# Kernel tuning notes

Hardware: AMD Instinct MI355X
Metric: run time of the kernel (lower is better)

The kernel has to match this reference:

```python
import jax, jax.numpy as jnp
import numpy as np

K = 3   # num nearest neighbors (init k)
P = 2   # IDW power (init p)


def setup_inputs() -> dict:
    key = jax.random.key(0)
    k1, k2, k3, k4 = jax.random.split(key, 4)
    B, N, M, C = 8, 16384, 1024, 256
    xyz = jax.random.normal(k1, (B, N, 3), dtype=jnp.float32)
    sampled_xyz = jax.random.normal(k2, (B, M, 3), dtype=jnp.float32)
    sampled_features = jax.random.normal(k3, (B, M, C), dtype=jnp.float32)
    masks = jax.random.randint(k4, (B, N), 0, 2, dtype=jnp.int32)
    return {"xyz": xyz, "sampled_xyz": sampled_xyz,
            "sampled_features": sampled_features, "masks": masks}


def reference(xyz, sampled_xyz, sampled_features, masks):
    # xyz: [B,N,3], sampled_xyz: [B,M,3], sampled_features: [B,M,C], masks: [B,N]
    # Squared pairwise distances [B,N,M] (same math as the chunked torch loop).
    delta = xyz[:, :, None, :] - sampled_xyz[:, None, :, :]
    dists = jnp.sum(delta * delta, axis=-1)
    # k smallest distances -> negate and take top-k.
    neg_top, idx = jax.lax.top_k(-dists, K)          # [B,N,K]
    min_dists = jnp.maximum(-neg_top, 1e-10)
    weights = 1.0 / (min_dists ** P + 1e-10)
    weights = weights / jnp.sum(weights, axis=-1, keepdims=True)
    # Gather neighbor features: [B,N,K,C]
    gathered = jax.vmap(lambda f, i: f[i])(sampled_features, idx)
    interpolated = jnp.sum(gathered * weights[..., None], axis=2)  # [B,N,C]
    # Invalid (masked-out) rows stay zero, matching the padded scatter.
    valid = (masks != 0).astype(interpolated.dtype)
    return interpolated * valid[..., None]
```

## Files before the change

### kernel.cpp

```cpp
#include <hip/hip_runtime.h>

constexpr int B = 8;
constexpr int N = 16384;
constexpr int M = 1024;
constexpr int C = 256;
constexpr int QW = 4;

typedef float vf16 __attribute__((ext_vector_type(16)));

__global__ __launch_bounds__(256, 8) void upsample_idw_kernel(
    const float* __restrict__ xyz,
    const float* __restrict__ sxyz,
    const float* __restrict__ feats,
    const int*   __restrict__ masks,
    float*       __restrict__ out)
{
    const int tid = threadIdx.x;
    const int w   = tid >> 6;
    const int l   = tid & 63;
    const int blk = blockIdx.x;
    const int b     = blk & 7;
    const int nbase = (blk >> 3) << 7;

    __shared__ unsigned long long s_key[2][64][QW][3];
    __shared__ float s_wt[2][64][3];
    __shared__ int   s_j[2][64][4];

    const float* bbase = sxyz + (size_t)b * (M * 3);
    const int qoff = __builtin_amdgcn_readfirstlane((tid >> 6) * (256 * 12));

    const float* xp0 = xyz + ((size_t)b * N + nbase + l) * 3;
    const float* xp1 = xyz + ((size_t)b * N + nbase + 64 + l) * 3;
    const float x0 = xp0[0], y0 = xp0[1], z0 = xp0[2];
    const float x1 = xp1[0], y1 = xp1[1], z1 = xp1[2];

    const float4* Fb4 = (const float4*)(feats + (size_t)b * (M * C));
    float4* op40 = (float4*)(out + (((size_t)b * N + nbase) * C));
    float4* op41 = (float4*)(out + (((size_t)b * N + nbase + 64) * C));

    auto scan_chunk = [&](int ch, float px, float py, float pz,
                          float& d0, float& d1, float& d2,
                          int& i0, int& i1, int& i2) {
        vf16 ca, cb, cc;
        const int off = qoff + ch * 192;
        asm volatile(
            "s_load_dwordx16 %0, %3, %4\n\t"
            "s_load_dwordx16 %1, %3, %4 offset:64\n\t"
            "s_load_dwordx16 %2, %3, %4 offset:128\n\t"
            "s_waitcnt lgkmcnt(0)"
            : "=&s"(ca), "=&s"(cb), "=&s"(cc)
            : "s"(bbase), "s"(off));
        #pragma unroll
        for (int j = 0; j < 16; ++j) {
            const int f0 = 3 * j, f1 = 3 * j + 1, f2 = 3 * j + 2;
            const float cx = (f0 < 16) ? ca[f0 & 15] : (f0 < 32) ? cb[f0 & 15] : cc[f0 & 15];
            const float cy = (f1 < 16) ? ca[f1 & 15] : (f1 < 32) ? cb[f1 & 15] : cc[f1 & 15];
            const float cz = (f2 < 16) ? ca[f2 & 15] : (f2 < 32) ? cb[f2 & 15] : cc[f2 & 15];
            const float dx = __fsub_rn(cx, px);
            const float dy = __fsub_rn(cy, py);
            const float dz = __fsub_rn(cz, pz);
            const float d  = __fadd_rn(__fadd_rn(__fmul_rn(dx, dx), __fmul_rn(dy, dy)),
                                       __fmul_rn(dz, dz));
            const int m = ch * 16 + j;
            const bool lt0 = d < d0, lt1 = d < d1, lt2 = d < d2;
            i2 = lt1 ? i1 : (lt2 ? m : i2);
            i1 = lt0 ? i0 : (lt1 ? m : i1);
            i0 = lt0 ? m  : i0;
            const float nd2 = __builtin_amdgcn_fmed3f(d1, d2, d);
            const float nd1 = __builtin_amdgcn_fmed3f(d0, d1, d);
            d2 = nd2; d1 = nd1; d0 = fminf(d0, d);
        }
    };

    auto store_keys = [&](int t, float d0, float d1, float d2,
                          int i0, int i1, int i2) {
        const unsigned base = (unsigned)(w * 256);
        s_key[t][l][w][0] = ((unsigned long long)__float_as_uint(d0) << 32) | (base + (unsigned)i0);
        s_key[t][l][w][1] = ((unsigned long long)__float_as_uint(d1) << 32) | (base + (unsigned)i1);
        s_key[t][l][w][2] = ((unsigned long long)__float_as_uint(d2) << 32) | (base + (unsigned)i2);
    };

    auto merge = [&](int t) {
        if (tid < 64) {
            unsigned long long k0 = ~0ULL, k1 = ~0ULL, k2 = ~0ULL;
            #pragma unroll
            for (int q = 0; q < QW; ++q) {
                #pragma unroll
                for (int s = 0; s < 3; ++s) {
                    const unsigned long long k = s_key[t][tid][q][s];
                    const bool lt0 = k < k0, lt1 = k < k1, lt2 = k < k2;
                    k2 = lt1 ? k1 : (lt2 ? k : k2);
                    k1 = lt0 ? k0 : (lt1 ? k : k1);
                    k0 = lt0 ? k  : k0;
                }
            }
            const float e0 = __uint_as_float((unsigned)(k0 >> 32));
            const float e1 = __uint_as_float((unsigned)(k1 >> 32));
            const float e2 = __uint_as_float((unsigned)(k2 >> 32));
            const float m0 = fmaxf(e0, 1e-10f);
            const float m1 = fmaxf(e1, 1e-10f);
            const float m2 = fmaxf(e2, 1e-10f);
            float w0 = 1.0f / (m0 * m0 + 1e-10f);
            float w1 = 1.0f / (m1 * m1 + 1e-10f);
            float w2 = 1.0f / (m2 * m2 + 1e-10f);
            const int valid = masks[(size_t)b * N + nbase + t * 64 + tid];
            const float scale = valid ? (1.0f / (w0 + w1 + w2)) : 0.0f;
            s_wt[t][tid][0] = w0 * scale;
            s_wt[t][tid][1] = w1 * scale;
            s_wt[t][tid][2] = w2 * scale;
            s_j[t][tid][0] = (int)(unsigned)k0;
            s_j[t][tid][1] = (int)(unsigned)k1;
            s_j[t][tid][2] = (int)(unsigned)k2;
            s_j[t][tid][3] = valid;
        }
    };

    auto phase2_iter = [&](int t, int i, float4* op4) {
        const int p = 4 * i + w;
        const int vld = __builtin_amdgcn_readfirstlane(s_j[t][p][3]);
        float4 acc = make_float4(0.f, 0.f, 0.f, 0.f);
        if (vld) {
            const int j0 = __builtin_amdgcn_readfirstlane(s_j[t][p][0]);
            const int j1 = __builtin_amdgcn_readfirstlane(s_j[t][p][1]);
            const int j2 = __builtin_amdgcn_readfirstlane(s_j[t][p][2]);
            const float u0 = __uint_as_float(
                __builtin_amdgcn_readfirstlane((int)__float_as_uint(s_wt[t][p][0])));
            const float u1 = __uint_as_float(
                __builtin_amdgcn_readfirstlane((int)__float_as_uint(s_wt[t][p][1])));
            const float u2 = __uint_as_float(
                __builtin_amdgcn_readfirstlane((int)__float_as_uint(s_wt[t][p][2])));
            const float4 f0 = Fb4[j0 * 64 + l];
            const float4 f1 = Fb4[j1 * 64 + l];
            const float4 f2 = Fb4[j2 * 64 + l];
            acc.x = fmaf(u2, f2.x, fmaf(u1, f1.x, u0 * f0.x));
            acc.y = fmaf(u2, f2.y, fmaf(u1, f1.y, u0 * f0.y));
            acc.z = fmaf(u2, f2.z, fmaf(u1, f1.z, u0 * f0.z));
            acc.w = fmaf(u2, f2.w, fmaf(u1, f1.w, u0 * f0.w));
        }
        op4[p * 64 + l] = acc;
    };

    {
        float d0 = __builtin_inff(), d1 = __builtin_inff(), d2 = __builtin_inff();
        int   i0 = 0, i1 = 0, i2 = 0;
        for (int ch = 0; ch < 16; ++ch)
            scan_chunk(ch, x0, y0, z0, d0, d1, d2, i0, i1, i2);
        store_keys(0, d0, d1, d2, i0, i1, i2);
    }
    __syncthreads();
    merge(0);
    __syncthreads();

    {
        float d0 = __builtin_inff(), d1 = __builtin_inff(), d2 = __builtin_inff();
        int   i0 = 0, i1 = 0, i2 = 0;
        for (int i = 0; i < 16; ++i) {
            phase2_iter(0, i, op40);
            scan_chunk(i, x1, y1, z1, d0, d1, d2, i0, i1, i2);
        }
        store_keys(1, d0, d1, d2, i0, i1, i2);
    }
    __syncthreads();
    merge(1);
    __syncthreads();

    for (int i = 0; i < 16; ++i)
        phase2_iter(1, i, op41);
}

extern "C" void kernel_launch(void* const* d_in, const int* in_sizes, int n_in,
                              void* d_out, int out_size, void* d_ws, size_t ws_size,
                              hipStream_t stream) {
    const float* xyz   = (const float*)d_in[0];
    const float* sxyz  = (const float*)d_in[1];
    const float* feats = (const float*)d_in[2];
    const int*   masks = (const int*)d_in[3];
    float*       out   = (float*)d_out;

    dim3 grid(B * N / 128);
    dim3 block(256);
    hipLaunchKernelGGL(upsample_idw_kernel, grid, block, 0, stream,
                       xyz, sxyz, feats, masks, out);
}
```

Before: 80.51 us.

## Split candidate scan across eight waves and software-pipeline feature gathers

The block grows from 256 to 512 threads, so eight waves each scan 128 of the 1024 sampled points per query instead of four waves scanning 256. The merge step now combines 24 partial top-3 candidates per query. The gather phase is restructured so feature loads for the next output row are issued before the current scan chunks run and consumed afterwards, which is meant to hide gather latency behind the distance scan. In exchange the merge is longer, register pressure rises from the values held across the pipeline, and launch_bounds(512,8) may constrain registers.

```diff
diff --git a/kernel.cpp b/kernel.cpp
--- a/kernel.cpp
+++ b/kernel.cpp
@@ -4,11 +4,10 @@
 constexpr int N = 16384;
 constexpr int M = 1024;
 constexpr int C = 256;
-constexpr int QW = 4;
 
-typedef float vf16 __attribute__((ext_vector_type(16)));
+typedef float vf8 __attribute__((ext_vector_type(8)));
 
-__global__ __launch_bounds__(256, 8) void upsample_idw_kernel(
+__global__ __launch_bounds__(512, 8) void upsample_idw_kernel(
     const float* __restrict__ xyz,
     const float* __restrict__ sxyz,
     const float* __restrict__ feats,
@@ -22,12 +21,12 @@
     const int b     = blk & 7;
     const int nbase = (blk >> 3) << 7;
 
-    __shared__ unsigned long long s_key[2][64][QW][3];
+    __shared__ unsigned long long s_key[64][25];
     __shared__ float s_wt[2][64][3];
-    __shared__ int   s_j[2][64][4];
+    __shared__ int   s_jv[2][64][4];
 
     const float* bbase = sxyz + (size_t)b * (M * 3);
-    const int qoff = __builtin_amdgcn_readfirstlane((tid >> 6) * (256 * 12));
+    const int qoff = __builtin_amdgcn_readfirstlane((tid >> 6) * 1536);
 
     const float* xp0 = xyz + ((size_t)b * N + nbase + l) * 3;
     const float* xp1 = xyz + ((size_t)b * N + nbase + 64 + l) * 3;
@@ -35,33 +34,38 @@
     const float x1 = xp1[0], y1 = xp1[1], z1 = xp1[2];
 
     const float4* Fb4 = (const float4*)(feats + (size_t)b * (M * C));
-    float4* op40 = (float4*)(out + (((size_t)b * N + nbase) * C));
-    float4* op41 = (float4*)(out + (((size_t)b * N + nbase + 64) * C));
+    float4* op4_0 = (float4*)(out + (((size_t)b * N + nbase) * C));
+    float4* op4_1 = (float4*)(out + (((size_t)b * N + nbase + 64) * C));
 
-    auto scan_chunk = [&](int ch, float px, float py, float pz,
-                          float& d0, float& d1, float& d2,
-                          int& i0, int& i1, int& i2) {
-        vf16 ca, cb, cc;
-        const int off = qoff + ch * 192;
+    float d0, d1, d2;
+    int   i0, i1, i2;
+    auto reset_ladder = [&]() {
+        d0 = d1 = d2 = __builtin_inff();
+        i0 = i1 = i2 = 0;
+    };
+
+    auto scan_chunk = [&](int ch, float px, float py, float pz) {
+        vf8 ca, cb, cc;
+        const int off = qoff + ch * 96;
         asm volatile(
-            "s_load_dwordx16 %0, %3, %4\n\t"
-            "s_load_dwordx16 %1, %3, %4 offset:64\n\t"
-            "s_load_dwordx16 %2, %3, %4 offset:128\n\t"
+            "s_load_dwordx8 %0, %3, %4\n\t"
+            "s_load_dwordx8 %1, %3, %4 offset:32\n\t"
+            "s_load_dwordx8 %2, %3, %4 offset:64\n\t"
             "s_waitcnt lgkmcnt(0)"
             : "=&s"(ca), "=&s"(cb), "=&s"(cc)
             : "s"(bbase), "s"(off));
         #pragma unroll
-        for (int j = 0; j < 16; ++j) {
+        for (int j = 0; j < 8; ++j) {
             const int f0 = 3 * j, f1 = 3 * j + 1, f2 = 3 * j + 2;
-            const float cx = (f0 < 16) ? ca[f0 & 15] : (f0 < 32) ? cb[f0 & 15] : cc[f0 & 15];
-            const float cy = (f1 < 16) ? ca[f1 & 15] : (f1 < 32) ? cb[f1 & 15] : cc[f1 & 15];
-            const float cz = (f2 < 16) ? ca[f2 & 15] : (f2 < 32) ? cb[f2 & 15] : cc[f2 & 15];
+            const float cx = (f0 < 8) ? ca[f0 & 7] : (f0 < 16) ? cb[f0 & 7] : cc[f0 & 7];
+            const float cy = (f1 < 8) ? ca[f1 & 7] : (f1 < 16) ? cb[f1 & 7] : cc[f1 & 7];
+            const float cz = (f2 < 8) ? ca[f2 & 7] : (f2 < 16) ? cb[f2 & 7] : cc[f2 & 7];
             const float dx = __fsub_rn(cx, px);
             const float dy = __fsub_rn(cy, py);
             const float dz = __fsub_rn(cz, pz);
             const float d  = __fadd_rn(__fadd_rn(__fmul_rn(dx, dx), __fmul_rn(dy, dy)),
                                        __fmul_rn(dz, dz));
-            const int m = ch * 16 + j;
+            const int m = ch * 8 + j;
             const bool lt0 = d < d0, lt1 = d < d1, lt2 = d < d2;
             i2 = lt1 ? i1 : (lt2 ? m : i2);
             i1 = lt0 ? i0 : (lt1 ? m : i1);
@@ -72,22 +76,21 @@
         }
     };
 
-    auto store_keys = [&](int t, float d0, float d1, float d2,
-                          int i0, int i1, int i2) {
-        const unsigned base = (unsigned)(w * 256);
-        s_key[t][l][w][0] = ((unsigned long long)__float_as_uint(d0) << 32) | (base + (unsigned)i0);
-        s_key[t][l][w][1] = ((unsigned long long)__float_as_uint(d1) << 32) | (base + (unsigned)i1);
-        s_key[t][l][w][2] = ((unsigned long long)__float_as_uint(d2) << 32) | (base + (unsigned)i2);
+    auto store_keys = [&]() {
+        const unsigned base = (unsigned)(w * 128);
+        s_key[l][w * 3 + 0] = ((unsigned long long)__float_as_uint(d0) << 32) | (base + (unsigned)i0);
+        s_key[l][w * 3 + 1] = ((unsigned long long)__float_as_uint(d1) << 32) | (base + (unsigned)i1);
+        s_key[l][w * 3 + 2] = ((unsigned long long)__float_as_uint(d2) << 32) | (base + (unsigned)i2);
     };
 
-    auto merge = [&](int t) {
+    auto merge_t = [&](int t) {
         if (tid < 64) {
             unsigned long long k0 = ~0ULL, k1 = ~0ULL, k2 = ~0ULL;
             #pragma unroll
-            for (int q = 0; q < QW; ++q) {
+            for (int q = 0; q < 8; ++q) {
                 #pragma unroll
                 for (int s = 0; s < 3; ++s) {
-                    const unsigned long long k = s_key[t][tid][q][s];
+                    const unsigned long long k = s_key[tid][q * 3 + s];
                     const bool lt0 = k < k0, lt1 = k < k1, lt2 = k < k2;
                     k2 = lt1 ? k1 : (lt2 ? k : k2);
                     k1 = lt0 ? k0 : (lt1 ? k : k1);
@@ -103,69 +106,80 @@
             float w0 = 1.0f / (m0 * m0 + 1e-10f);
             float w1 = 1.0f / (m1 * m1 + 1e-10f);
             float w2 = 1.0f / (m2 * m2 + 1e-10f);
-            const int valid = masks[(size_t)b * N + nbase + t * 64 + tid];
+            const int valid = masks[(size_t)b * N + nbase + t * 64 + tid] ? 1 : 0;
             const float scale = valid ? (1.0f / (w0 + w1 + w2)) : 0.0f;
             s_wt[t][tid][0] = w0 * scale;
             s_wt[t][tid][1] = w1 * scale;
             s_wt[t][tid][2] = w2 * scale;
-            s_j[t][tid][0] = (int)(unsigned)k0;
-            s_j[t][tid][1] = (int)(unsigned)k1;
-            s_j[t][tid][2] = (int)(unsigned)k2;
-            s_j[t][tid][3] = valid;
+            s_jv[t][tid][0] = (int)(unsigned)k0;
+            s_jv[t][tid][1] = (int)(unsigned)k1;
+            s_jv[t][tid][2] = (int)(unsigned)k2;
+            s_jv[t][tid][3] = valid;
         }
     };
 
-    auto phase2_iter = [&](int t, int i, float4* op4) {
-        const int p = 4 * i + w;
-        const int vld = __builtin_amdgcn_readfirstlane(s_j[t][p][3]);
-        float4 acc = make_float4(0.f, 0.f, 0.f, 0.f);
-        if (vld) {
-            const int j0 = __builtin_amdgcn_readfirstlane(s_j[t][p][0]);
-            const int j1 = __builtin_amdgcn_readfirstlane(s_j[t][p][1]);
-            const int j2 = __builtin_amdgcn_readfirstlane(s_j[t][p][2]);
-            const float u0 = __uint_as_float(
-                __builtin_amdgcn_readfirstlane((int)__float_as_uint(s_wt[t][p][0])));
-            const float u1 = __uint_as_float(
-                __builtin_amdgcn_readfirstlane((int)__float_as_uint(s_wt[t][p][1])));
-            const float u2 = __uint_as_float(
-                __builtin_amdgcn_readfirstlane((int)__float_as_uint(s_wt[t][p][2])));
-            const float4 f0 = Fb4[j0 * 64 + l];
-            const float4 f1 = Fb4[j1 * 64 + l];
-            const float4 f2 = Fb4[j2 * 64 + l];
-            acc.x = fmaf(u2, f2.x, fmaf(u1, f1.x, u0 * f0.x));
-            acc.y = fmaf(u2, f2.y, fmaf(u1, f1.y, u0 * f0.y));
-            acc.z = fmaf(u2, f2.z, fmaf(u1, f1.z, u0 * f0.z));
-            acc.w = fmaf(u2, f2.w, fmaf(u1, f1.w, u0 * f0.w));
+    float4 ga, gb, gc;
+    float  ua, ub, uc;
+    int    prow = 0, pval = 0;
+
+    auto p2_issue = [&](int t, int i) {
+        const int rg = tid >> 6;
+        const int cq = tid & 63;
+        prow = i * 8 + rg;
+        pval = __builtin_amdgcn_readfirstlane(s_jv[t][prow][3]);
+        if (pval) {
+            const int j0 = __builtin_amdgcn_readfirstlane(s_jv[t][prow][0]);
+            const int j1 = __builtin_amdgcn_readfirstlane(s_jv[t][prow][1]);
+            const int j2 = __builtin_amdgcn_readfirstlane(s_jv[t][prow][2]);
+            ua = __uint_as_float((unsigned)
+                __builtin_amdgcn_readfirstlane((int)__float_as_uint(s_wt[t][prow][0])));
+            ub = __uint_as_float((unsigned)
+                __builtin_amdgcn_readfirstlane((int)__float_as_uint(s_wt[t][prow][1])));
+            uc = __uint_as_float((unsigned)
+                __builtin_amdgcn_readfirstlane((int)__float_as_uint(s_wt[t][prow][2])));
+            ga = Fb4[j0 * 64 + cq];
+            gb = Fb4[j1 * 64 + cq];
+            gc = Fb4[j2 * 64 + cq];
         }
-        op4[p * 64 + l] = acc;
     };
 
-    {
-        float d0 = __builtin_inff(), d1 = __builtin_inff(), d2 = __builtin_inff();
-        int   i0 = 0, i1 = 0, i2 = 0;
-        for (int ch = 0; ch < 16; ++ch)
-            scan_chunk(ch, x0, y0, z0, d0, d1, d2, i0, i1, i2);
-        store_keys(0, d0, d1, d2, i0, i1, i2);
-    }
+    auto p2_consume = [&](float4* op4t) {
+        const int cq = tid & 63;
+        float4 acc = make_float4(0.f, 0.f, 0.f, 0.f);
+        if (pval) {
+            acc.x = fmaf(uc, gc.x, fmaf(ub, gb.x, ua * ga.x));
+            acc.y = fmaf(uc, gc.y, fmaf(ub, gb.y, ua * ga.y));
+            acc.z = fmaf(uc, gc.z, fmaf(ub, gb.z, ua * ga.z));
+            acc.w = fmaf(uc, gc.w, fmaf(ub, gb.w, ua * ga.w));
+        }
+        op4t[prow * 64 + cq] = acc;
+    };
+
+    reset_ladder();
+    for (int ch = 0; ch < 16; ++ch)
+        scan_chunk(ch, x0, y0, z0);
+    store_keys();
     __syncthreads();
-    merge(0);
+    merge_t(0);
     __syncthreads();
 
-    {
-        float d0 = __builtin_inff(), d1 = __builtin_inff(), d2 = __builtin_inff();
-        int   i0 = 0, i1 = 0, i2 = 0;
-        for (int i = 0; i < 16; ++i) {
-            phase2_iter(0, i, op40);
-            scan_chunk(i, x1, y1, z1, d0, d1, d2, i0, i1, i2);
-        }
-        store_keys(1, d0, d1, d2, i0, i1, i2);
+    reset_ladder();
+    p2_issue(0, 0);
+    for (int i = 0; i < 8; ++i) {
+        scan_chunk(2 * i,     x1, y1, z1);
+        scan_chunk(2 * i + 1, x1, y1, z1);
+        p2_consume(op4_0);
+        if (i < 7) p2_issue(0, i + 1);
     }
+    store_keys();
     __syncthreads();
-    merge(1);
+    merge_t(1);
     __syncthreads();
 
-    for (int i = 0; i < 16; ++i)
-        phase2_iter(1, i, op41);
+    for (int i = 0; i < 8; ++i) {
+        p2_issue(1, i);
+        p2_consume(op4_1);
+    }
 }
 
 extern "C" void kernel_launch(void* const* d_in, const int* in_sizes, int n_in,
@@ -178,7 +192,7 @@
     float*       out   = (float*)d_out;
 
     dim3 grid(B * N / 128);
-    dim3 block(256);
+    dim3 block(512);
     hipLaunchKernelGGL(upsample_idw_kernel, grid, block, 0, stream,
                        xyz, sxyz, feats, masks, out);
 }
```

Result: faster. 78.32 us (-2.7%).
